# Performance work log

Measured on AMD Instinct MI355X. Metric: run time of the kernel, lower is better.

The kernel has to match this reference:

```python
import jax, jax.numpy as jnp
import numpy as np

T = 37          # bio_type_num
LP = T + 2      # padded label size (start, end)
START, END = T, T + 1


def crf_loglik(logits, labels, lens, trans):
    # logits: [B,S,LP] padded scores; labels: [B,S] ints; lens: [B]; trans[to, from]: [LP,LP]
    B, S, Lp = logits.shape
    dt = logits.dtype
    tpos = jnp.arange(S)
    mask = (tpos[None, :] < lens[:, None]).astype(dt)  # [B,S]
    # unary gold score
    unary = jnp.take_along_axis(logits, labels[..., None], axis=2)[..., 0] * mask
    # binary (transition) gold score with start/end extension
    labels_ext = jnp.concatenate([
        jnp.full((B, 1), START, labels.dtype), labels, jnp.full((B, 1), END, labels.dtype)], axis=1)  # [B,S+2]
    pos = jnp.arange(S + 2)
    labels_ext = jnp.where(pos[None, :] < (lens + 1)[:, None], labels_ext, END)
    frm, to = labels_ext[:, :-1], labels_ext[:, 1:]          # [B,S+1]
    trn_scr = trans[to, frm]                                  # [B,S+1]
    m2 = (jnp.arange(S + 1)[None, :] < (lens + 1)[:, None]).astype(dt)
    gold = unary.sum(1) + (trn_scr * m2).sum(1)               # [B]
    # partition function: forward algorithm (sequential scan over time)
    alpha0 = jnp.full((B, Lp), -100.0, dt).at[:, START].set(0.0)
    def step(alpha, xt):
        logit_t, m_t = xt                                     # [B,Lp], [B] bool
        mat = logit_t[:, :, None] + alpha[:, None, :] + trans[None, :, :]  # [B,to,from]
        alpha_nxt = jax.nn.logsumexp(mat, axis=2)
        alpha = jnp.where(m_t[:, None], alpha_nxt, alpha)
        return alpha, None
    xs = (jnp.swapaxes(logits, 0, 1), (tpos[None, :] < lens[:, None]).T)
    alpha, _ = jax.lax.scan(step, alpha0, xs)
    alpha = alpha + trans[END][None, :]
    norm = jax.nn.logsumexp(alpha, axis=1)                    # [B]
    return gold - norm


def ner_forward(h, bio_embed, W_cat, b_cat, W_crf, b_crf, transition, token_nums, entity_seq_labels):
    B, S, H = h.shape
    scale = 1.0 / jnp.sqrt(jnp.asarray(H, h.dtype))
    # one-head attention: query=token states, key=value=bio type embeddings (mask all ones -> no-op)
    scores = jnp.einsum('bsh,th->bst', h, bio_embed) * scale  # [B,S,T]
    attn = jax.nn.softmax(scores, axis=-1)
    aware = jnp.einsum('bst,th->bsh', attn, bio_embed)        # [B,S,H]
    x = jnp.concatenate([h, aware, h * aware], axis=-1)       # [B,S,3H]
    x = jax.nn.gelu(x @ W_cat + b_cat, approximate=False)     # [B,S,H]
    logits = x @ W_crf + b_crf                                # [B,S,T]
    pads = jnp.full((B, S, 2), -10000.0, logits.dtype)
    ner_scores = jnp.concatenate([logits, pads], axis=-1)     # [B,S,LP]
    ner_loss = crf_loglik(ner_scores, entity_seq_labels, token_nums, transition)
    return ner_scores, ner_loss


def setup_inputs() -> dict:
    key = jax.random.key(0)
    ks = jax.random.split(key, 8)
    B, S, H = 32, 512, 1024
    token_hidden_states = jax.random.normal(ks[0], (B, S, H), jnp.float32)
    token_masks = jnp.ones((B, S), jnp.bool_)
    token_nums = jax.random.randint(ks[1], (B,), 256, S + 1).at[0].set(S)
    entity_seq_labels = jax.random.randint(ks[2], (B, S), 0, T)
    bio_embed = jax.random.normal(ks[3], (T, H), jnp.float32) * 0.02
    W_cat = jax.random.normal(ks[4], (3 * H, H), jnp.float32) * (3.0 * H) ** -0.5
    b_cat = jnp.zeros((H,), jnp.float32)
    W_crf = jax.random.normal(ks[5], (H, T), jnp.float32) * H ** -0.5
    b_crf = jnp.zeros((T,), jnp.float32)
    transition = jax.random.normal(ks[6], (LP, LP), jnp.float32)
    return {
        'token_hidden_states': token_hidden_states, 'token_masks': token_masks,
        'token_nums': token_nums, 'entity_seq_labels': entity_seq_labels,
        'bio_embed': bio_embed, 'W_cat': W_cat, 'b_cat': b_cat,
        'W_crf': W_crf, 'b_crf': b_crf, 'transition': transition,
    }


def reference(token_hidden_states, token_masks, token_nums, entity_seq_labels,
              bio_embed, W_cat, b_cat, W_crf, b_crf, transition):
    # token_masks only generates an all-ones bio mask in the original (no-op); dropout in eval mode.
    return ner_forward(token_hidden_states, bio_embed, W_cat, b_cat, W_crf, b_crf,
                       transition, token_nums, entity_seq_labels)
```

## Files before the change

kernel.cpp:

```cpp
#include <hip/hip_runtime.h>
#include <hip/hip_bf16.h>
#include <math.h>

#define NB 32
#define NS 512
#define NH 1024
#define NT 37
#define NLP 39
#define NM (NB*NS)

typedef __attribute__((ext_vector_type(8))) short bf16x8;
typedef __attribute__((ext_vector_type(4))) float f32x4;

__device__ __forceinline__ float bf2f(unsigned int u) {
    unsigned int x = u << 16;
    float f;
    __builtin_memcpy(&f, &x, 4);
    return f;
}
__device__ __forceinline__ unsigned short f2bf(float f) {
    __hip_bfloat16 hb = __float2bfloat16(f);
    unsigned short u;
    __builtin_memcpy(&u, &hb, 2);
    return u;
}
__device__ __forceinline__ unsigned int pk2(float lo, float hi) {
    return ((unsigned int)f2bf(hi) << 16) | (unsigned int)f2bf(lo);
}
__device__ __forceinline__ int SW64(int b)  { return b ^ ((b >> 2) & 0x70); }
__device__ __forceinline__ int TSW(int row, int kcolByte) {
    return (row * 128 + kcolByte) ^ ((row & 7) << 4);
}
__device__ __forceinline__ float rl(float x, int l) {
    return __int_as_float(__builtin_amdgcn_readlane(__float_as_int(x), l));
}
__device__ __forceinline__ void gld16(const void* g, void* l) {
    __builtin_amdgcn_global_load_lds((const __attribute__((address_space(1))) void*)g,
                                     (__attribute__((address_space(3))) void*)l, 16, 0, 0);
}
#define VMW(N) asm volatile("s_waitcnt vmcnt(" #N ")" ::: "memory")
#define BARR() do { __builtin_amdgcn_s_barrier(); __builtin_amdgcn_sched_barrier(0); } while (0)

__global__ __launch_bounds__(512) void kA1(const float* __restrict__ h,
                                           const float* __restrict__ bio,
                                           unsigned short* __restrict__ attn) {
    __shared__ __align__(16) char Bl[48 * 2048];

    const int tid  = threadIdx.x;
    const int lane = tid & 63;
    const int wid  = tid >> 6;
    const int lr   = lane & 15;
    const int lk   = lane >> 4;
    const int m0   = blockIdx.x * 128;

    for (int idx = tid; idx < 37 * 256; idx += 512) {
        int t = idx >> 8, k4 = idx & 255;
        float4 v = *(const float4*)&bio[(size_t)t * NH + k4 * 4];
        int byte = (t * 2048 + k4 * 8) ^ ((t & 7) << 4);
        *(uint2*)(Bl + byte) = make_uint2(pk2(v.x, v.y), pk2(v.z, v.w));
    }
    for (int idx = tid; idx < 11 * 256; idx += 512) {
        int t = 37 + (idx >> 8), k4 = idx & 255;
        int byte = (t * 2048 + k4 * 8) ^ ((t & 7) << 4);
        *(uint2*)(Bl + byte) = make_uint2(0, 0);
    }
    __syncthreads();

    const int arow = m0 + wid * 16 + lr;
    const float* hp = h + (size_t)arow * NH + lk * 8;

    f32x4 sacc[3];
#pragma unroll
    for (int j = 0; j < 3; ++j) sacc[j] = (f32x4){0.f, 0.f, 0.f, 0.f};

    float4 p0 = *(const float4*)(hp);
    float4 p1 = *(const float4*)(hp + 4);
    for (int kt = 0; kt < NH; kt += 32) {
        float4 c0 = p0, c1 = p1;
        if (kt + 32 < NH) {
            p0 = *(const float4*)(hp + kt + 32);
            p1 = *(const float4*)(hp + kt + 36);
        }
        union { unsigned int u[4]; bf16x8 v; } af;
        af.u[0] = pk2(c0.x, c0.y); af.u[1] = pk2(c0.z, c0.w);
        af.u[2] = pk2(c1.x, c1.y); af.u[3] = pk2(c1.z, c1.w);
#pragma unroll
        for (int nf = 0; nf < 3; ++nf) {
            int t = nf * 16 + lr;
            int byte = (t * 2048 + (kt + lk * 8) * 2) ^ ((t & 7) << 4);
            bf16x8 bf = *(const bf16x8*)(Bl + byte);
            sacc[nf] = __builtin_amdgcn_mfma_f32_16x16x32_bf16(af.v, bf, sacc[nf], 0, 0, 0);
        }
    }

#pragma unroll
    for (int r = 0; r < 4; ++r) {
        const int orow = wid * 16 + lk * 4 + r;
        float s0 = sacc[0][r] * 0.03125f;
        float s1 = sacc[1][r] * 0.03125f;
        float s2 = sacc[2][r] * 0.03125f;
        const bool v2 = (lr < 5);
        float mx = fmaxf(fmaxf(s0, s1), v2 ? s2 : -1e30f);
#pragma unroll
        for (int d = 1; d < 16; d <<= 1) mx = fmaxf(mx, __shfl_xor(mx, d, 64));
        float e0 = __expf(s0 - mx), e1 = __expf(s1 - mx);
        float e2 = v2 ? __expf(s2 - mx) : 0.f;
        float sm = e0 + e1 + e2;
#pragma unroll
        for (int d = 1; d < 16; d <<= 1) sm += __shfl_xor(sm, d, 64);
        float inv = 1.f / sm;
        size_t g = (size_t)(m0 + orow) * 64;
        attn[g + lr]      = f2bf(e0 * inv);
        attn[g + 16 + lr] = f2bf(e1 * inv);
        attn[g + 32 + lr] = f2bf(e2 * inv);
        attn[g + 48 + lr] = 0;
    }
}

__global__ __launch_bounds__(256) void kA2(const unsigned short* __restrict__ attn,
                                           const float* __restrict__ bio,
                                           unsigned short* __restrict__ aware) {
    __shared__ __align__(16) char Bsl[128 * 64];

    const int tid  = threadIdx.x;
    const int lane = tid & 63;
    const int wid  = tid >> 6;
    const int wm   = (wid >> 1) * 64;
    const int wn   = (wid & 1) * 64;
    const int lr   = lane & 15;
    const int lk   = lane >> 4;
    const int n0   = blockIdx.x * 128;
    const int m0   = blockIdx.y * 128;

    const int bn = tid & 127;
    const int bq = (tid >> 7) * 16;

    f32x4 acc[4][4];
#pragma unroll
    for (int i = 0; i < 4; ++i)
#pragma unroll
        for (int j = 0; j < 4; ++j) acc[i][j] = (f32x4){0.f, 0.f, 0.f, 0.f};

#pragma unroll
    for (int ks = 0; ks < 2; ++ks) {
        unsigned int p[8];
#pragma unroll
        for (int i = 0; i < 8; ++i) {
            int t0 = ks*32 + bq + 2*i;
            float lo = (t0     < NT) ? bio[(size_t)t0 * NH + n0 + bn]       : 0.f;
            float hi = (t0 + 1 < NT) ? bio[(size_t)(t0+1) * NH + n0 + bn]   : 0.f;
            p[i] = pk2(lo, hi);
        }
        __syncthreads();
        *(int4*)(Bsl + SW64(bn*64 + bq*2))      = make_int4(p[0], p[1], p[2], p[3]);
        *(int4*)(Bsl + SW64(bn*64 + bq*2 + 16)) = make_int4(p[4], p[5], p[6], p[7]);
        __syncthreads();

        bf16x8 af[4];
#pragma unroll
        for (int mf = 0; mf < 4; ++mf)
            af[mf] = *(const bf16x8*)(attn + (size_t)(m0 + wm + mf*16 + lr) * 64 + ks*32 + lk*8);
#pragma unroll
        for (int nf = 0; nf < 4; ++nf) {
            bf16x8 bb = *(const bf16x8*)(Bsl + SW64((wn + nf*16 + lr)*64 + lk*16));
#pragma unroll
            for (int mf = 0; mf < 4; ++mf)
                acc[mf][nf] = __builtin_amdgcn_mfma_f32_16x16x32_bf16(af[mf], bb, acc[mf][nf], 0, 0, 0);
        }
    }

#pragma unroll
    for (int mf = 0; mf < 4; ++mf)
#pragma unroll
        for (int nf = 0; nf < 4; ++nf)
#pragma unroll
            for (int r = 0; r < 4; ++r) {
                size_t row = (size_t)(m0 + wm + mf*16 + lk*4 + r);
                aware[row * NH + n0 + wn + nf*16 + lr] = f2bf(acc[mf][nf][r]);
            }
}

__global__ __launch_bounds__(256) void kA2f(const unsigned short* __restrict__ attn,
                                            const float* __restrict__ bio,
                                            const float* __restrict__ h,
                                            char* __restrict__ Asw) {
    __shared__ __align__(16) char Bsl[128 * 64];
    __shared__ __align__(16) unsigned short awL[128 * 128];

    const int tid  = threadIdx.x;
    const int lane = tid & 63;
    const int wid  = tid >> 6;
    const int wm   = (wid >> 1) * 64;
    const int wn   = (wid & 1) * 64;
    const int lr   = lane & 15;
    const int lk   = lane >> 4;
    const int n0   = blockIdx.x * 128;
    const int m0   = blockIdx.y * 128;
    const int tm   = blockIdx.y;

    const int bn = tid & 127;
    const int bq = (tid >> 7) * 16;

    f32x4 acc[4][4];
#pragma unroll
    for (int i = 0; i < 4; ++i)
#pragma unroll
        for (int j = 0; j < 4; ++j) acc[i][j] = (f32x4){0.f, 0.f, 0.f, 0.f};

#pragma unroll
    for (int ks = 0; ks < 2; ++ks) {
        unsigned int p[8];
#pragma unroll
        for (int i = 0; i < 8; ++i) {
            int t0 = ks*32 + bq + 2*i;
            float lo = (t0     < NT) ? bio[(size_t)t0 * NH + n0 + bn]       : 0.f;
            float hi = (t0 + 1 < NT) ? bio[(size_t)(t0+1) * NH + n0 + bn]   : 0.f;
            p[i] = pk2(lo, hi);
        }
        __syncthreads();
        *(int4*)(Bsl + SW64(bn*64 + bq*2))      = make_int4(p[0], p[1], p[2], p[3]);
        *(int4*)(Bsl + SW64(bn*64 + bq*2 + 16)) = make_int4(p[4], p[5], p[6], p[7]);
        __syncthreads();

        bf16x8 af[4];
#pragma unroll
        for (int mf = 0; mf < 4; ++mf)
            af[mf] = *(const bf16x8*)(attn + (size_t)(m0 + wm + mf*16 + lr) * 64 + ks*32 + lk*8);
#pragma unroll
        for (int nf = 0; nf < 4; ++nf) {
            bf16x8 bb = *(const bf16x8*)(Bsl + SW64((wn + nf*16 + lr)*64 + lk*16));
#pragma unroll
            for (int mf = 0; mf < 4; ++mf)
                acc[mf][nf] = __builtin_amdgcn_mfma_f32_16x16x32_bf16(af[mf], bb, acc[mf][nf], 0, 0, 0);
        }
    }

#pragma unroll
    for (int mf = 0; mf < 4; ++mf)
#pragma unroll
        for (int nf = 0; nf < 4; ++nf)
#pragma unroll
            for (int r = 0; r < 4; ++r)
                awL[(wm + mf*16 + lk*4 + r) * 128 + wn + nf*16 + lr] = f2bf(acc[mf][nf][r]);
    __syncthreads();

#pragma unroll
    for (int i = 0; i < 8; ++i) {
        int lin = tid + i * 256;
        int row = lin >> 4, kg = lin & 15;
        uint4 v = *(const uint4*)&awL[row * 128 + kg * 8];
        int kglob = 1024 + n0 + kg * 8;
        size_t tbase = ((size_t)tm * 48 + (kglob >> 6)) * 16384;
        *(uint4*)(Asw + tbase + TSW(row, (kglob & 63) * 2)) = v;
    }
#pragma unroll
    for (int i = 0; i < 8; ++i) {
        int lin = tid + i * 256;
        int row = lin >> 4, kg = lin & 15;
        const float4* hp = (const float4*)&h[(size_t)(m0 + row) * NH + n0 + kg * 8];
        float4 ha = hp[0], hb = hp[1];
        float hv[8] = {ha.x, ha.y, ha.z, ha.w, hb.x, hb.y, hb.z, hb.w};
        uint4 awv = *(const uint4*)&awL[row * 128 + kg * 8];
        unsigned int awu[4] = {awv.x, awv.y, awv.z, awv.w};
        unsigned int p0[4], p2[4];
#pragma unroll
        for (int j = 0; j < 4; ++j) {
            p0[j] = pk2(hv[2*j], hv[2*j+1]);
            float lo = hv[2*j]   * bf2f(awu[j] & 0xffffu);
            float hi = hv[2*j+1] * bf2f(awu[j] >> 16);
            p2[j] = pk2(lo, hi);
        }
        int k0g = n0 + kg * 8;
        size_t tb0 = ((size_t)tm * 48 + (k0g >> 6)) * 16384;
        *(uint4*)(Asw + tb0 + TSW(row, (k0g & 63) * 2)) = make_uint4(p0[0], p0[1], p0[2], p0[3]);
        int k2g = 2048 + n0 + kg * 8;
        size_t tb2 = ((size_t)tm * 48 + (k2g >> 6)) * 16384;
        *(uint4*)(Asw + tb2 + TSW(row, (k2g & 63) * 2)) = make_uint4(p2[0], p2[1], p2[2], p2[3]);
    }
}

__global__ __launch_bounds__(256) void kW(const float* __restrict__ Wcat,
                                          char* __restrict__ Wsw) {
    __shared__ unsigned short wt[64 * 128];

    const int tid  = threadIdx.x;
    const int tile = blockIdx.x;
    const int tn   = tile / 48;
    const int tk   = tile - tn * 48;
    const int n00  = tn * 128;
    const int k0   = tk * 64;

#pragma unroll
    for (int i = 0; i < 8; ++i) {
        int lin = tid + i * 256;
        int kk = lin >> 5, ng = lin & 31;
        float4 v = *(const float4*)&Wcat[(size_t)(k0 + kk) * NH + n00 + ng * 4];
        unsigned int lo = pk2(v.x, v.y), hi = pk2(v.z, v.w);
        *(uint2*)&wt[kk * 128 + ng * 4] = make_uint2(lo, hi);
    }
    __syncthreads();
#pragma unroll
    for (int i = 0; i < 4; ++i) {
        int lin = tid + i * 256;
        int rn = lin >> 3, kg = lin & 7;
        unsigned short t8[8];
#pragma unroll
        for (int j = 0; j < 8; ++j) t8[j] = wt[(kg * 8 + j) * 128 + rn];
        uint4 v = *(const uint4*)t8;
        *(uint4*)(Wsw + (size_t)tile * 16384 + TSW(rn, kg * 16)) = v;
    }
}

__global__ __launch_bounds__(256) void kW2(const float* __restrict__ Wcrf,
                                           unsigned short* __restrict__ WT) {
    const int idx = blockIdx.x * 256 + threadIdx.x;
    if (idx >= 48 * 384) return;
    const int t = idx / 384, kg = idx - t * 384;
    unsigned short v[8];
#pragma unroll
    for (int e = 0; e < 8; ++e) {
        int k = kg * 8 + e;
        v[e] = (t < NT) ? f2bf(Wcrf[(size_t)k * NT + t]) : (unsigned short)0;
    }
    uint4 w;
    __builtin_memcpy(&w, v, 16);
    *(uint4*)(WT + (size_t)t * 3072 + kg * 8) = w;
}

__global__ __launch_bounds__(512, 2) void kBf(const char* __restrict__ Asw,
                                              const char* __restrict__ Wsw,
                                              const float* __restrict__ bcat,
                                              const unsigned short* __restrict__ WT,
                                              float* __restrict__ P) {
    __shared__ __align__(16) char lds[131072];

    const int tid  = threadIdx.x;
    const int lane = tid & 63;
    const int wid  = tid >> 6;
    const int widm = wid >> 2;
    const int widn = wid & 3;
    const int lr   = lane & 15;
    const int lk   = lane >> 4;

    const int id   = blockIdx.x;
    const int xcd  = id & 7;
    const int slot = id >> 3;
    const int Mt   = xcd * 8 + (slot >> 2);
    const int Nt   = slot & 3;
    const int m0   = Mt * 256, n0 = Nt * 256;
    const int soff = tid * 16;

    f32x4 acc00[4][2], acc01[4][2], acc10[4][2], acc11[4][2];
#pragma unroll
    for (int i = 0; i < 4; ++i)
#pragma unroll
        for (int j = 0; j < 2; ++j) {
            acc00[i][j] = (f32x4){0.f,0.f,0.f,0.f};
            acc01[i][j] = (f32x4){0.f,0.f,0.f,0.f};
            acc10[i][j] = (f32x4){0.f,0.f,0.f,0.f};
            acc11[i][j] = (f32x4){0.f,0.f,0.f,0.f};
        }

    auto stageHalf = [&](int T, int ph) {
        const bool isA = (ph == 0) || (ph == 3);
        const int  h   = isA ? (ph == 3 ? 1 : 0) : (ph - 1);
        const char* src = isA
            ? Asw + ((size_t)((2*Mt + h) * 48 + T)) * 16384
            : Wsw + ((size_t)((2*Nt + h) * 48 + T)) * 16384;
        char* dst = lds + (isA ? 0 : 65536) + (T & 1) * 32768 + h * 16384;
        gld16(src + soff,        dst + soff);
        gld16(src + soff + 8192, dst + soff + 8192);
    };
    auto loadA = [&](bf16x8 (&af)[4][2], int q, int half) {
        const char* base = lds + q * 32768 + half * 16384;
#pragma unroll
        for (int i = 0; i < 4; ++i) {
            int row = widm * 64 + i * 16 + lr;
#pragma unroll
            for (int kk = 0; kk < 2; ++kk)
                af[i][kk] = *(const bf16x8*)(base + TSW(row, kk * 64 + lk * 16));
        }
    };
    auto loadB = [&](bf16x8 (&bfr)[2][2], int q, int half) {
        const char* base = lds + 65536 + q * 32768 + half * 16384;
#pragma unroll
        for (int j = 0; j < 2; ++j) {
            int col = widn * 32 + j * 16 + lr;
#pragma unroll
            for (int kk = 0; kk < 2; ++kk)
                bfr[j][kk] = *(const bf16x8*)(base + TSW(col, kk * 64 + lk * 16));
        }
    };
    auto mma = [&](f32x4 (&ac)[4][2], bf16x8 (&af)[4][2], bf16x8 (&bfr)[2][2]) {
        __builtin_amdgcn_s_setprio(1);
#pragma unroll
        for (int kk = 0; kk < 2; ++kk)
#pragma unroll
            for (int i = 0; i < 4; ++i)
#pragma unroll
                for (int j = 0; j < 2; ++j)
                    ac[i][j] = __builtin_amdgcn_mfma_f32_16x16x32_bf16(
                        af[i][kk], bfr[j][kk], ac[i][j], 0, 0, 0);
        __builtin_amdgcn_s_setprio(0);
    };

    stageHalf(0, 0); stageHalf(0, 1); stageHalf(0, 2); stageHalf(0, 3);
    VMW(0);
    BARR();

    for (int T = 0; T < 47; ++T) {
        const int q = T & 1;
        bf16x8 af0[4][2], af1[4][2], bf0[2][2], bf1[2][2];
        stageHalf(T + 1, 0);
        VMW(6);
        BARR();
        loadA(af0, q, 0); loadB(bf0, q, 0);
        mma(acc00, af0, bf0);
        stageHalf(T + 1, 1);
        VMW(6);
        BARR();
        loadB(bf1, q, 1);
        mma(acc01, af0, bf1);
        stageHalf(T + 1, 2);
        VMW(6);
        BARR();
        loadA(af1, q, 1);
        mma(acc10, af1, bf0);
        stageHalf(T + 1, 3);
        BARR();
        mma(acc11, af1, bf1);
    }
    {
        const int q = 1;
        bf16x8 af0[4][2], af1[4][2], bf0[2][2], bf1[2][2];
        VMW(4);
        BARR();
        loadA(af0, q, 0); loadB(bf0, q, 0);
        mma(acc00, af0, bf0);
        VMW(2);
        BARR();
        loadB(bf1, q, 1);
        mma(acc01, af0, bf1);
        VMW(0);
        BARR();
        loadA(af1, q, 1);
        mma(acc10, af1, bf0);
        BARR();
        mma(acc11, af1, bf1);
    }

    __syncthreads();
    auto stashQ = [&](f32x4 (&ac)[4][2], int a, int b) {
#pragma unroll
        for (int j = 0; j < 2; ++j) {
            const int lcol = b * 128 + widn * 32 + j * 16 + lr;
            const int kc = lcol >> 6, kk = lcol & 63;
            const float bc = bcat[n0 + lcol];
#pragma unroll
            for (int i = 0; i < 4; ++i)
#pragma unroll
                for (int r = 0; r < 4; ++r) {
                    int lrow = a * 128 + widm * 64 + i * 16 + lk * 4 + r;
                    float x = ac[i][j][r] + bc;
                    float g = 0.5f * x * (1.0f + erff(x * 0.70710678118654752f));
                    *(unsigned short*)(lds + kc * 32768 + TSW(lrow, kk * 2)) = f2bf(g);
                }
        }
    };
    stashQ(acc00, 0, 0); stashQ(acc01, 0, 1); stashQ(acc10, 1, 0); stashQ(acc11, 1, 1);
    __syncthreads();

    bf16x8 wfrag[3][8];
#pragma unroll
    for (int tt = 0; tt < 3; ++tt) {
        const int t = tt * 16 + lr;
#pragma unroll
        for (int ks = 0; ks < 8; ++ks)
            wfrag[tt][ks] = *(const bf16x8*)(WT + (size_t)t * 3072 + n0 + ks * 32 + lk * 8);
    }

    f32x4 pacc[2][3];
#pragma unroll
    for (int i = 0; i < 2; ++i)
#pragma unroll
        for (int j = 0; j < 3; ++j) pacc[i][j] = (f32x4){0.f, 0.f, 0.f, 0.f};
#pragma unroll
    for (int rt2 = 0; rt2 < 2; ++rt2) {
        const int lrow = wid * 32 + rt2 * 16 + lr;
#pragma unroll
        for (int ks = 0; ks < 8; ++ks) {
            const int kc = ks >> 1, kh = ks & 1;
            bf16x8 af = *(const bf16x8*)(lds + kc * 32768 + TSW(lrow, kh * 64 + lk * 16));
#pragma unroll
            for (int tt = 0; tt < 3; ++tt)
                pacc[rt2][tt] = __builtin_amdgcn_mfma_f32_16x16x32_bf16(
                    af, wfrag[tt][ks], pacc[rt2][tt], 0, 0, 0);
        }
    }

    float* Pb = P + (size_t)Nt * NM * 48;
#pragma unroll
    for (int rt2 = 0; rt2 < 2; ++rt2)
#pragma unroll
        for (int tt = 0; tt < 3; ++tt)
#pragma unroll
            for (int r = 0; r < 4; ++r) {
                int row = Mt * 256 + wid * 32 + rt2 * 16 + lk * 4 + r;
                Pb[(size_t)row * 48 + tt * 16 + lr] = pacc[rt2][tt][r];
            }
}

__global__ __launch_bounds__(256) void kCr(const float* __restrict__ P,
                                           const float* __restrict__ bcrf,
                                           float* __restrict__ out) {
    const int g = blockIdx.x * 256 + threadIdx.x;
    const size_t STRIDE = (size_t)NM * 48;
#pragma unroll
    for (int s = 0; s < 12; ++s) {
        int flat = g * 12 + s;
        int row = flat / 48, t = flat - row * 48;
        float v = P[flat] + P[STRIDE + flat] + P[2*STRIDE + flat] + P[3*STRIDE + flat];
        if (t < NT)       out[(size_t)row * NLP + t] = v + bcrf[t];
        else if (t < NLP) out[(size_t)row * NLP + t] = -10000.0f;
    }
}

__global__ __launch_bounds__(64) void kDm(const float* __restrict__ scores,
                                          const int* __restrict__ lens,
                                          const float* __restrict__ trans,
                                          float* __restrict__ Pm,
                                          float* __restrict__ Pc) {
    __shared__ float el_all[64 * 64];
    __shared__ __align__(16) char Mb[2 * 6144];

    const int lane = threadIdx.x;
    const int b    = blockIdx.x >> 3;
    const int s    = blockIdx.x & 7;
    const int lr   = lane & 15;
    const int lk   = lane >> 4;
    const int len  = lens[b];
    const int t0   = s * 64;
    const int nsteps = (len > t0) ? ((len - t0 < 64) ? (len - t0) : 64) : 0;
    const float* sb = scores + (size_t)b * NS * NLP;
    float* Pg = Pm + (size_t)(b * 8 + s) * 2304;

    if (nsteps == 0) {
        for (int j = 0; j < 36; ++j) {
            int flat = j * 64 + lane;
            Pg[flat] = 0.f;
        }
        if (lane < 48) Pg[lane * 48 + lane] = (lane < NLP) ? 1.f : 1.f;
        if (lane == 0) Pc[b * 8 + s] = 0.f;
        return;
    }

    for (int i = 0; i < 64; ++i) {
        float v = 0.f;
        if (i < nsteps && lane < NLP) v = __expf(sb[(size_t)(t0 + i) * NLP + lane]);
        el_all[i * 64 + lane] = v;
    }

    bf16x8 Tf[3][2];
#pragma unroll
    for (int tt = 0; tt < 3; ++tt)
#pragma unroll
        for (int ks = 0; ks < 2; ++ks) {
            const int row = tt * 16 + lr;
            unsigned int u[4];
#pragma unroll
            for (int e2 = 0; e2 < 4; ++e2) {
                int f0 = ks * 32 + lk * 8 + 2 * e2;
                float lo = (row < NLP && f0     < NLP) ? __expf(trans[row * NLP + f0])     : 0.f;
                float hi = (row < NLP && f0 + 1 < NLP) ? __expf(trans[row * NLP + f0 + 1]) : 0.f;
                u[e2] = pk2(lo, hi);
            }
            union { unsigned int uu[4]; bf16x8 v; } cv;
            cv.uu[0]=u[0]; cv.uu[1]=u[1]; cv.uu[2]=u[2]; cv.uu[3]=u[3];
            Tf[tt][ks] = cv.v;
        }

    for (int j = 0; j < 48; ++j)
        *(unsigned int*)(Mb + j * 256 + lane * 4) = 0;
    if (lane < 48) {
        int byte = (lane * 128 + lane * 2) ^ ((lane & 7) << 4);
        *(unsigned short*)(Mb + byte) = f2bf(1.0f);
    }

    float Cacc = 0.f;

    for (int i = 0; i < nsteps; ++i) {
        const int q = i & 1;
        const char* Mr = Mb + q * 6144;

        bf16x8 Bf[3][2];
#pragma unroll
        for (int ct = 0; ct < 3; ++ct) {
#pragma unroll
            for (int ks = 0; ks < 2; ++ks) {
                int col = ct * 16 + lr;
                int byte = (col * 128 + (ks * 32 + lk * 8) * 2) ^ ((col & 7) << 4);
                Bf[ct][ks] = *(const bf16x8*)(Mr + byte);
            }
        }
        f32x4 el4[3];
#pragma unroll
        for (int tt = 0; tt < 3; ++tt)
            el4[tt] = *(const f32x4*)&el_all[i * 64 + tt * 16 + lk * 4];

        f32x4 c[3][3];
#pragma unroll
        for (int tt = 0; tt < 3; ++tt)
#pragma unroll
            for (int ct = 0; ct < 3; ++ct) {
                c[tt][ct] = __builtin_amdgcn_mfma_f32_16x16x32_bf16(
                    Tf[tt][0], Bf[ct][0], (f32x4){0.f,0.f,0.f,0.f}, 0, 0, 0);
                c[tt][ct] = __builtin_amdgcn_mfma_f32_16x16x32_bf16(
                    Tf[tt][1], Bf[ct][1], c[tt][ct], 0, 0, 0);
            }
#pragma unroll
        for (int tt = 0; tt < 3; ++tt)
#pragma unroll
            for (int ct = 0; ct < 3; ++ct)
#pragma unroll
                for (int r = 0; r < 4; ++r)
                    c[tt][ct][r] *= el4[tt][r];

        if ((i & 3) == 3) {
            float sv = rl(c[0][0][0], 0);
            float rr = __builtin_amdgcn_rcpf(sv);
#pragma unroll
            for (int tt = 0; tt < 3; ++tt)
#pragma unroll
                for (int ct = 0; ct < 3; ++ct)
#pragma unroll
                    for (int r = 0; r < 4; ++r) c[tt][ct][r] *= rr;
            Cacc -= __logf(rr);
        }

        if (i == nsteps - 1) {
#pragma unroll
            for (int tt = 0; tt < 3; ++tt)
#pragma unroll
                for (int ct = 0; ct < 3; ++ct)
#pragma unroll
                    for (int r = 0; r < 4; ++r) {
                        int row = tt * 16 + lk * 4 + r;
                        int col = ct * 16 + lr;
                        Pg[row * 48 + col] = c[tt][ct][r];
                    }
        } else {
            char* Mw = Mb + (q ^ 1) * 6144;
#pragma unroll
            for (int tt = 0; tt < 3; ++tt)
#pragma unroll
                for (int ct = 0; ct < 3; ++ct) {
                    int col = ct * 16 + lr;
                    int k   = tt * 16 + lk * 4;
                    int byte = (col * 128 + k * 2) ^ ((col & 7) << 4);
                    *(uint2*)(Mw + byte) = make_uint2(pk2(c[tt][ct][0], c[tt][ct][1]),
                                                      pk2(c[tt][ct][2], c[tt][ct][3]));
                }
        }
    }

    if (lane == 0) Pc[b * 8 + s] = Cacc;
}

__global__ __launch_bounds__(256) void kDc(const float* __restrict__ scores,
                                           const int* __restrict__ labels,
                                           const int* __restrict__ lens,
                                           const float* __restrict__ trans,
                                           const float* __restrict__ Pm,
                                           const float* __restrict__ Pc,
                                           float* __restrict__ loss) {
    __shared__ float trL[39 * 41];
    __shared__ float gred[4];

    const int b    = blockIdx.x;
    const int tid  = threadIdx.x;
    const int lane = tid & 63;
    const int wid  = tid >> 6;
    const int len  = lens[b];
    const float* sb = scores + (size_t)b * NS * NLP;

    for (int idx = tid; idx < 39 * 39; idx += 256) {
        int to = idx / 39, f = idx - to * 39;
        trL[to * 41 + f] = trans[idx];
    }
    __syncthreads();

    float g = 0.0f;
    for (int t = tid; t < len; t += 256) g += sb[(size_t)t * NLP + labels[b * NS + t]];
    for (int i = tid; i <= len; i += 256) {
        int frm = (i == 0) ? 37 : labels[b * NS + i - 1];
        int to  = (i == len) ? 38 : labels[b * NS + i];
        g += trL[to * 41 + frm];
    }
#pragma unroll
    for (int off = 32; off > 0; off >>= 1) g += __shfl_xor(g, off, 64);
    if (lane == 0) gred[wid] = g;
    __syncthreads();

    if (wid != 0) return;

    const float gold = (gred[0] + gred[1]) + (gred[2] + gred[3]);
    const bool act48 = (lane < 48);

    const float* P0 = Pm + (size_t)b * 8 * 2304;
    float v = act48 ? P0[lane * 48 + 37] : 0.f;
    float C = Pc[b * 8];

    for (int s = 1; s < 8; ++s) {
        float as_[40];
#pragma unroll
        for (int f = 0; f < 40; ++f) as_[f] = rl(v, f);
        __builtin_amdgcn_sched_barrier(0);
        const float* Ps = Pm + (size_t)(b * 8 + s) * 2304;
        float c = 0.f;
        if (act48) {
            const float4* rowp = (const float4*)(Ps + lane * 48);
#pragma unroll
            for (int q = 0; q < 10; ++q) {
                float4 rv = rowp[q];
                c = fmaf(rv.x, as_[q*4+0], c);
                c = fmaf(rv.y, as_[q*4+1], c);
                c = fmaf(rv.z, as_[q*4+2], c);
                c = fmaf(rv.w, as_[q*4+3], c);
            }
        }
        float sv = rl(c, 0);
        float rr = __builtin_amdgcn_rcpf(sv);
        v = c * rr;
        C -= __logf(rr);
        C += Pc[b * 8 + s];
    }

    const float trEnd = (lane < NLP) ? trL[38 * 41 + lane] : 0.f;
    float aend = (lane < NLP && v > 0.f) ? C + __logf(v) + trEnd : -1e30f;
    float mx = aend;
#pragma unroll
    for (int off = 32; off > 0; off >>= 1) mx = fmaxf(mx, __shfl_xor(mx, off, 64));
    float es = (lane < NLP) ? __expf(aend - mx) : 0.f;
#pragma unroll
    for (int off = 32; off > 0; off >>= 1) es += __shfl_xor(es, off, 64);
    float norm = mx + __logf(es);

    if (lane == 0) loss[b] = gold - norm;
}

__global__ __launch_bounds__(256) void kB(const float* __restrict__ h,
                                          const unsigned short* __restrict__ aware,
                                          const float* __restrict__ Wcat,
                                          const float* __restrict__ bcat,
                                          unsigned short* __restrict__ x2) {
    __shared__ __align__(16) char lds[16384];
    char* Asl = lds;
    char* Bsl = lds + 8192;

    const int tid  = threadIdx.x;
    const int lane = tid & 63;
    const int wid  = tid >> 6;
    const int wm   = (wid >> 1) * 64;
    const int wn   = (wid & 1) * 64;
    const int lr   = lane & 15;
    const int lk   = lane >> 4;

    const int id   = blockIdx.x;
    const int xcd  = id & 7;
    const int slot = id >> 3;
    const int m0   = (xcd * 16 + (slot >> 3)) * 128;
    const int n0   = (slot & 7) * 128;

    const int am = tid >> 1;
    const int ak = (tid & 1) * 16;
    const int bn = tid & 127;
    const int bk = (tid >> 7) * 16;

    f32x4 acc[4][4];
#pragma unroll
    for (int i = 0; i < 4; ++i)
#pragma unroll
        for (int j = 0; j < 4; ++j) acc[i][j] = (f32x4){0.f, 0.f, 0.f, 0.f};

    const float*          hrow = h     + (size_t)(m0 + am) * NH + ak;
    const unsigned short* arow = aware + (size_t)(m0 + am) * NH + ak;
    const float*          wcol = Wcat  + (size_t)bk * NH + n0 + bn;

    float hv[16];
    unsigned int aw[8];
    float wv[16];

    auto stage = [&](int kt) {
        const int region = kt >> 10;
        const int kb = kt & 1023;
        if (region != 1) {
            const float4* hp = (const float4*)(hrow + kb);
            float4 a = hp[0], b = hp[1], c = hp[2], d = hp[3];
            hv[0]=a.x; hv[1]=a.y; hv[2]=a.z; hv[3]=a.w;
            hv[4]=b.x; hv[5]=b.y; hv[6]=b.z; hv[7]=b.w;
            hv[8]=c.x; hv[9]=c.y; hv[10]=c.z; hv[11]=c.w;
            hv[12]=d.x; hv[13]=d.y; hv[14]=d.z; hv[15]=d.w;
        }
        if (region >= 1) {
            const uint4* ap = (const uint4*)(arow + kb);
            uint4 a0 = ap[0], a1 = ap[1];
            aw[0]=a0.x; aw[1]=a0.y; aw[2]=a0.z; aw[3]=a0.w;
            aw[4]=a1.x; aw[5]=a1.y; aw[6]=a1.z; aw[7]=a1.w;
        }
        {
            const float* wp = wcol + (size_t)kt * NH;
#pragma unroll
            for (int j = 0; j < 16; ++j) wv[j] = wp[(size_t)j * NH];
        }
    };

    auto writeStage = [&](int kt) {
        const int region = kt >> 10;
        unsigned int p[8];
        if (region == 0) {
#pragma unroll
            for (int i = 0; i < 8; ++i) p[i] = pk2(hv[2*i], hv[2*i+1]);
        } else if (region == 1) {
#pragma unroll
            for (int i = 0; i < 8; ++i) p[i] = aw[i];
        } else {
#pragma unroll
            for (int i = 0; i < 8; ++i) {
                float lo = hv[2*i]   * bf2f(aw[i] & 0xffffu);
                float hi = hv[2*i+1] * bf2f(aw[i] >> 16);
                p[i] = pk2(lo, hi);
            }
        }
        *(int4*)(Asl + SW64(am*64 + ak*2))      = make_int4(p[0], p[1], p[2], p[3]);
        *(int4*)(Asl + SW64(am*64 + ak*2 + 16)) = make_int4(p[4], p[5], p[6], p[7]);
        unsigned int q[8];
#pragma unroll
        for (int i = 0; i < 8; ++i) q[i] = pk2(wv[2*i], wv[2*i+1]);
        *(int4*)(Bsl + SW64(bn*64 + bk*2))      = make_int4(q[0], q[1], q[2], q[3]);
        *(int4*)(Bsl + SW64(bn*64 + bk*2 + 16)) = make_int4(q[4], q[5], q[6], q[7]);
    };

    stage(0);
    for (int kt = 0; kt < 3072; kt += 32) {
        __syncthreads();
        writeStage(kt);
        __syncthreads();
        if (kt + 32 < 3072) stage(kt + 32);

        bf16x8 af[4], bfr[4];
#pragma unroll
        for (int mf = 0; mf < 4; ++mf)
            af[mf] = *(const bf16x8*)(Asl + SW64((wm + mf*16 + lr)*64 + lk*16));
#pragma unroll
        for (int nf = 0; nf < 4; ++nf)
            bfr[nf] = *(const bf16x8*)(Bsl + SW64((wn + nf*16 + lr)*64 + lk*16));
#pragma unroll
        for (int mf = 0; mf < 4; ++mf)
#pragma unroll
            for (int nf = 0; nf < 4; ++nf)
                acc[mf][nf] = __builtin_amdgcn_mfma_f32_16x16x32_bf16(af[mf], bfr[nf], acc[mf][nf], 0, 0, 0);
    }

#pragma unroll
    for (int nf = 0; nf < 4; ++nf) {
        const int col = n0 + wn + nf*16 + lr;
        const float bc = bcat[col];
#pragma unroll
        for (int mf = 0; mf < 4; ++mf)
#pragma unroll
            for (int r = 0; r < 4; ++r) {
                size_t row = (size_t)(m0 + wm + mf*16 + lk*4 + r);
                float x = acc[mf][nf][r] + bc;
                float g = 0.5f * x * (1.0f + erff(x * 0.70710678118654752f));
                x2[row * NH + col] = f2bf(g);
            }
    }
}

__global__ __launch_bounds__(256) void kC(const unsigned short* __restrict__ x2,
                                          const float* __restrict__ Wcrf,
                                          const float* __restrict__ bcrf,
                                          float* __restrict__ out) {
    __shared__ __align__(16) char Asl[8192];
    __shared__ __align__(16) char Bsl[3072];

    const int tid  = threadIdx.x;
    const int lane = tid & 63;
    const int wid  = tid >> 6;
    const int lr   = lane & 15;
    const int lk   = lane >> 4;
    const int m0   = blockIdx.x * 128;
    const int am   = tid >> 1;
    const int ak   = (tid & 1) * 16;

    for (int i = tid; i < 192; i += 256) *(int4*)(Bsl + i*16) = make_int4(0, 0, 0, 0);

    f32x4 acc[2][3];
#pragma unroll
    for (int i = 0; i < 2; ++i)
#pragma unroll
        for (int j = 0; j < 3; ++j) acc[i][j] = (f32x4){0.f, 0.f, 0.f, 0.f};

    const unsigned short* xrow = x2 + (size_t)(m0 + am) * NH + ak;

    for (int kt = 0; kt < NH; kt += 32) {
        const uint4* xp = (const uint4*)(xrow + kt);
        uint4 x0 = xp[0], x1 = xp[1];
        float wv[5];
#pragma unroll
        for (int p = 0; p < 5; ++p) {
            int i = tid + p * 256;
            wv[p] = (i < 32*NT) ? Wcrf[(size_t)kt * NT + i] : 0.f;
        }
        __syncthreads();
        *(uint4*)(Asl + SW64(am*64 + ak*2))      = x0;
        *(uint4*)(Asl + SW64(am*64 + ak*2 + 16)) = x1;
#pragma unroll
        for (int p = 0; p < 5; ++p) {
            int i = tid + p * 256;
            if (i < 32*NT) {
                int kk = i / NT;
                int t  = i - kk * NT;
                *(unsigned short*)(Bsl + SW64(t*64 + kk*2)) = f2bf(wv[p]);
            }
        }
        __syncthreads();
        bf16x8 af[2], bfr[3];
#pragma unroll
        for (int mf = 0; mf < 2; ++mf)
            af[mf] = *(const bf16x8*)(Asl + SW64((wid*32 + mf*16 + lr)*64 + lk*16));
#pragma unroll
        for (int nf = 0; nf < 3; ++nf)
            bfr[nf] = *(const bf16x8*)(Bsl + SW64((nf*16 + lr)*64 + lk*16));
#pragma unroll
        for (int mf = 0; mf < 2; ++mf)
#pragma unroll
            for (int nf = 0; nf < 3; ++nf)
                acc[mf][nf] = __builtin_amdgcn_mfma_f32_16x16x32_bf16(af[mf], bfr[nf], acc[mf][nf], 0, 0, 0);
    }

#pragma unroll
    for (int nf = 0; nf < 3; ++nf) {
        const int t = nf*16 + lr;
        const float bc = (t < NT) ? bcrf[t] : 0.f;
#pragma unroll
        for (int mf = 0; mf < 2; ++mf)
#pragma unroll
            for (int r = 0; r < 4; ++r) {
                size_t row = (size_t)(m0 + wid*32 + mf*16 + lk*4 + r);
                if (t < NT)       out[row * NLP + t] = acc[mf][nf][r] + bc;
                else if (t < NLP) out[row * NLP + t] = -10000.0f;
            }
    }
}

#define CRFSTEP(EL) do {                                   \
    float as_[37];                                         \
    _Pragma("unroll")                                      \
    for (int f_ = 0; f_ < 37; ++f_) as_[f_] = rl(a, f_);   \
    __builtin_amdgcn_sched_barrier(0);                     \
    float c0 = 0.f, c1 = 0.f, c2 = 0.f, c3 = 0.f;          \
    _Pragma("unroll")                                      \
    for (int f_ = 0; f_ < 36; f_ += 4) {                   \
        c0 = fmaf(as_[f_    ], trow[f_    ], c0);          \
        c1 = fmaf(as_[f_ + 1], trow[f_ + 1], c1);          \
        c2 = fmaf(as_[f_ + 2], trow[f_ + 2], c2);          \
        c3 = fmaf(as_[f_ + 3], trow[f_ + 3], c3);          \
    }                                                      \
    c0 = fmaf(as_[36], trow[36], c0);                      \
    a = (EL) * ((c0 + c1) + (c2 + c3));                    \
} while (0)

__global__ __launch_bounds__(256) void kDold(const float* __restrict__ scores,
                                             const int* __restrict__ labels,
                                             const int* __restrict__ lens,
                                             const float* __restrict__ trans,
                                             float* __restrict__ loss) {
    __shared__ float S[NS * NLP];
    __shared__ float trL[39 * 41];
    __shared__ int   labL[NS];
    __shared__ float gred[4];

    const int b    = blockIdx.x;
    const int tid  = threadIdx.x;
    const int lane = tid & 63;
    const int wid  = tid >> 6;
    const int len  = lens[b];
    const float* sb = scores + (size_t)b * NS * NLP;

    {
        const int n4 = (len * NLP + 3) >> 2;
        const float4* src = (const float4*)sb;
        float4* dst = (float4*)S;
        for (int i = tid; i < n4; i += 256) dst[i] = src[i];
    }
    for (int i = tid; i < NS; i += 256) labL[i] = labels[b * NS + i];
    for (int idx = tid; idx < 39 * 39; idx += 256) {
        int to = idx / 39, f = idx - to * 39;
        trL[to * 41 + f] = trans[idx];
    }
    __syncthreads();

    float g = 0.0f;
    for (int t = tid; t < len; t += 256) g += S[t * NLP + labL[t]];
    for (int i = tid; i <= len; i += 256) {
        int frm = (i == 0) ? 37 : labL[i - 1];
        int to  = (i == len) ? 38 : labL[i];
        g += trL[to * 41 + frm];
    }
#pragma unroll
    for (int off = 32; off > 0; off >>= 1) g += __shfl_xor(g, off, 64);
    if (lane == 0) gred[wid] = g;
    __syncthreads();

    if (wid != 0) return;

    const float gold = (gred[0] + gred[1]) + (gred[2] + gred[3]);

    const int myrow = (lane < 39) ? lane : 0;
    float trow[39];
#pragma unroll
    for (int f = 0; f < 39; ++f) trow[f] = __expf(trL[myrow * 41 + f]);
    const float trEnd = (lane < 39) ? trL[38 * 41 + lane] : 0.f;
    const bool act = (lane < 39);

    float l0 = act ? S[lane] : -10000.f;
    float a = act ? __expf(l0) * trow[37] : 0.f;
    float C = 0.0f;

    auto ldrow = [&](int r) {
        r = (r < len) ? r : (len - 1);
        return S[act ? (r * NLP + lane) : 0];
    };
    float lg0 = ldrow(1), lg1 = ldrow(2), lg2 = ldrow(3), lg3 = ldrow(4);

    int t = 1;
    for (; t + 3 < len; t += 4) {
        float e0 = __expf(lg0), e1 = __expf(lg1), e2 = __expf(lg2), e3 = __expf(lg3);
        lg0 = ldrow(t + 4); lg1 = ldrow(t + 5); lg2 = ldrow(t + 6); lg3 = ldrow(t + 7);
        CRFSTEP(e0); CRFSTEP(e1); CRFSTEP(e2); CRFSTEP(e3);
        float s = rl(a, 0);
        float rr = __builtin_amdgcn_rcpf(s);
        a *= rr; C -= __logf(rr);
    }
    for (; t < len; ++t) {
        float el = __expf(ldrow(t));
        CRFSTEP(el);
    }

    float aend = (act && a > 0.f) ? C + __logf(a) + trEnd : -1e30f;
    float mx = aend;
#pragma unroll
    for (int off = 32; off > 0; off >>= 1) mx = fmaxf(mx, __shfl_xor(mx, off, 64));
    float es = act ? __expf(aend - mx) : 0.0f;
#pragma unroll
    for (int off = 32; off > 0; off >>= 1) es += __shfl_xor(es, off, 64);
    float norm = mx + __logf(es);

    if (lane == 0) loss[b] = gold - norm;
}

extern "C" void kernel_launch(void* const* d_in, const int* in_sizes, int n_in,
                              void* d_out, int out_size, void* d_ws, size_t ws_size,
                              hipStream_t stream) {
    const float* h        = (const float*)d_in[0];
    const int* token_nums = (const int*)d_in[2];
    const int* labels     = (const int*)d_in[3];
    const float* bio      = (const float*)d_in[4];
    const float* Wcat     = (const float*)d_in[5];
    const float* bcat     = (const float*)d_in[6];
    const float* Wcrf     = (const float*)d_in[7];
    const float* bcrf     = (const float*)d_in[8];
    const float* trans    = (const float*)d_in[9];

    float* out = (float*)d_out;
    unsigned short* attn  = (unsigned short*)d_out;

    const size_t ASW_BYTES = (size_t)128 * 48 * 16384;
    const size_t P_BYTES   = (size_t)4 * NM * 48 * 4;
    const size_t WSW_BYTES = (size_t)8 * 48 * 16384;
    const size_t WT_BYTES  = (size_t)48 * 3072 * 2;
    const size_t PM_BYTES  = (size_t)NB * 8 * 2304 * 4;
    const size_t PC_BYTES  = (size_t)NB * 8 * 4;
    const bool fast = ws_size >= ASW_BYTES + P_BYTES + WSW_BYTES + WT_BYTES + PM_BYTES + PC_BYTES;

    hipLaunchKernelGGL(kA1, dim3(NM / 128), dim3(512), 0, stream, h, bio, attn);

    if (fast) {
        char*  Asw = (char*)d_ws;
        float* P   = (float*)((char*)d_ws + ASW_BYTES);
        char*  Wsw = (char*)d_ws + ASW_BYTES + P_BYTES;
        unsigned short* WT = (unsigned short*)((char*)d_ws + ASW_BYTES + P_BYTES + WSW_BYTES);
        float* Pm  = (float*)((char*)d_ws + ASW_BYTES + P_BYTES + WSW_BYTES + WT_BYTES);
        float* Pc  = Pm + (size_t)NB * 8 * 2304;

        hipLaunchKernelGGL(kW, dim3(8 * 48), dim3(256), 0, stream, Wcat, Wsw);
        hipLaunchKernelGGL(kW2, dim3(72), dim3(256), 0, stream, Wcrf, WT);
        hipLaunchKernelGGL(kA2f, dim3(NH / 128, NM / 128), dim3(256), 0, stream,
                           attn, bio, h, Asw);
        hipLaunchKernelGGL(kBf, dim3(256), dim3(512), 0, stream, Asw, Wsw, bcat, WT, P);
        hipLaunchKernelGGL(kCr, dim3(256), dim3(256), 0, stream, P, bcrf, out);
        hipLaunchKernelGGL(kDm, dim3(NB * 8), dim3(64), 0, stream, out, token_nums, trans,
                           Pm, Pc);
        hipLaunchKernelGGL(kDc, dim3(NB), dim3(256), 0, stream, out, labels, token_nums,
                           trans, Pm, Pc, out + (size_t)NM * NLP);
    } else {
        unsigned short* aware = (unsigned short*)d_ws;
        unsigned short* x2    = aware + (size_t)NM * NH;

        hipLaunchKernelGGL(kA2, dim3(NH / 128, NM / 128), dim3(256), 0, stream, attn, bio, aware);
        hipLaunchKernelGGL(kB, dim3((NH / 128) * (NM / 128)), dim3(256), 0, stream,
                           h, aware, Wcat, bcat, x2);
        hipLaunchKernelGGL(kC, dim3(NM / 128), dim3(256), 0, stream, x2, Wcrf, bcrf, out);
        hipLaunchKernelGGL(kDold, dim3(NB), dim3(256), 0, stream, out, labels, token_nums,
                           trans, out + (size_t)NM * NLP);
    }
}
```

Measured before the change: 244.7 us.

## Merge attention-score, weight-prep kernels into one launch and reuse bf16 h from workspace

Three launches (attention-score softmax, Wcat swizzle, Wcrf transpose) become one kernel, kPre, that picks its role from the block index. The score part also writes the bf16 copy of h into the swizzled A workspace while it streams h. kA2f then reads that bf16 copy instead of reloading fp32 h, which removes one full fp32 read of h and two launches. The h*aware product is now formed from bf16-rounded h rather than fp32 h, which changes rounding slightly.

```diff
diff --git a/kernel.cpp b/kernel.cpp
--- a/kernel.cpp
+++ b/kernel.cpp
@@ -40,6 +40,134 @@
 }
 #define VMW(N) asm volatile("s_waitcnt vmcnt(" #N ")" ::: "memory")
 #define BARR() do { __builtin_amdgcn_s_barrier(); __builtin_amdgcn_sched_barrier(0); } while (0)
+
+__global__ __launch_bounds__(512) void kPre(const float* __restrict__ h,
+                                            const float* __restrict__ bio,
+                                            const float* __restrict__ Wcat,
+                                            const float* __restrict__ Wcrf,
+                                            unsigned short* __restrict__ attn,
+                                            char* __restrict__ Asw,
+                                            char* __restrict__ Wsw,
+                                            unsigned short* __restrict__ WT) {
+    __shared__ __align__(16) char shmem[48 * 2048];
+    const int bid = blockIdx.x;
+    const int tid = threadIdx.x;
+
+    if (bid < 128) {
+        char* Bl = shmem;
+        const int lane = tid & 63;
+        const int wid  = tid >> 6;
+        const int lr   = lane & 15;
+        const int lk   = lane >> 4;
+        const int m0   = bid * 128;
+
+        for (int idx = tid; idx < 37 * 256; idx += 512) {
+            int t = idx >> 8, k4 = idx & 255;
+            float4 v = *(const float4*)&bio[(size_t)t * NH + k4 * 4];
+            int byte = (t * 2048 + k4 * 8) ^ ((t & 7) << 4);
+            *(uint2*)(Bl + byte) = make_uint2(pk2(v.x, v.y), pk2(v.z, v.w));
+        }
+        for (int idx = tid; idx < 11 * 256; idx += 512) {
+            int t = 37 + (idx >> 8), k4 = idx & 255;
+            int byte = (t * 2048 + k4 * 8) ^ ((t & 7) << 4);
+            *(uint2*)(Bl + byte) = make_uint2(0, 0);
+        }
+        __syncthreads();
+
+        const int arow = m0 + wid * 16 + lr;
+        const float* hp = h + (size_t)arow * NH + lk * 8;
+        const int trow = wid * 16 + lr;
+
+        f32x4 sacc[3];
+#pragma unroll
+        for (int j = 0; j < 3; ++j) sacc[j] = (f32x4){0.f, 0.f, 0.f, 0.f};
+
+        float4 p0 = *(const float4*)(hp);
+        float4 p1 = *(const float4*)(hp + 4);
+        for (int kt = 0; kt < NH; kt += 32) {
+            float4 c0 = p0, c1 = p1;
+            if (kt + 32 < NH) {
+                p0 = *(const float4*)(hp + kt + 32);
+                p1 = *(const float4*)(hp + kt + 36);
+            }
+            union { unsigned int u[4]; bf16x8 v; uint4 q; } af;
+            af.u[0] = pk2(c0.x, c0.y); af.u[1] = pk2(c0.z, c0.w);
+            af.u[2] = pk2(c1.x, c1.y); af.u[3] = pk2(c1.z, c1.w);
+            {
+                int kg = kt + lk * 8;
+                size_t tb = ((size_t)bid * 48 + (kg >> 6)) * 16384;
+                *(uint4*)(Asw + tb + TSW(trow, (kg & 63) * 2)) = af.q;
+            }
+#pragma unroll
+            for (int nf = 0; nf < 3; ++nf) {
+                int t = nf * 16 + lr;
+                int byte = (t * 2048 + (kt + lk * 8) * 2) ^ ((t & 7) << 4);
+                bf16x8 bf = *(const bf16x8*)(Bl + byte);
+                sacc[nf] = __builtin_amdgcn_mfma_f32_16x16x32_bf16(af.v, bf, sacc[nf], 0, 0, 0);
+            }
+        }
+
+#pragma unroll
+        for (int r = 0; r < 4; ++r) {
+            const int orow = wid * 16 + lk * 4 + r;
+            float s0 = sacc[0][r] * 0.03125f;
+            float s1 = sacc[1][r] * 0.03125f;
+            float s2 = sacc[2][r] * 0.03125f;
+            const bool v2 = (lr < 5);
+            float mx = fmaxf(fmaxf(s0, s1), v2 ? s2 : -1e30f);
+#pragma unroll
+            for (int d = 1; d < 16; d <<= 1) mx = fmaxf(mx, __shfl_xor(mx, d, 64));
+            float e0 = __expf(s0 - mx), e1 = __expf(s1 - mx);
+            float e2 = v2 ? __expf(s2 - mx) : 0.f;
+            float sm = e0 + e1 + e2;
+#pragma unroll
+            for (int d = 1; d < 16; d <<= 1) sm += __shfl_xor(sm, d, 64);
+            float inv = 1.f / sm;
+            size_t g = (size_t)(m0 + orow) * 64;
+            attn[g + lr]      = f2bf(e0 * inv);
+            attn[g + 16 + lr] = f2bf(e1 * inv);
+            attn[g + 32 + lr] = f2bf(e2 * inv);
+            attn[g + 48 + lr] = 0;
+        }
+    } else if (bid < 512) {
+        unsigned short* wt = (unsigned short*)shmem;
+        const int tile = bid - 128;
+        const int tn   = tile / 48;
+        const int tk   = tile - tn * 48;
+        const int n00  = tn * 128;
+        const int k0   = tk * 64;
+
+        for (int lin = tid; lin < 2048; lin += 512) {
+            int kk = lin >> 5, ng = lin & 31;
+            float4 v = *(const float4*)&Wcat[(size_t)(k0 + kk) * NH + n00 + ng * 4];
+            *(uint2*)&wt[kk * 128 + ng * 4] = make_uint2(pk2(v.x, v.y), pk2(v.z, v.w));
+        }
+        __syncthreads();
+        for (int lin = tid; lin < 1024; lin += 512) {
+            int rn = lin >> 3, kg = lin & 7;
+            unsigned short t8[8];
+#pragma unroll
+            for (int j = 0; j < 8; ++j) t8[j] = wt[(kg * 8 + j) * 128 + rn];
+            uint4 v;
+            __builtin_memcpy(&v, t8, 16);
+            *(uint4*)(Wsw + (size_t)tile * 16384 + TSW(rn, kg * 16)) = v;
+        }
+    } else {
+        const int idx = (bid - 512) * 512 + tid;
+        if (idx < 48 * 384) {
+            const int t = idx / 384, kg = idx - t * 384;
+            unsigned short v[8];
+#pragma unroll
+            for (int e = 0; e < 8; ++e) {
+                int k = kg * 8 + e;
+                v[e] = (t < NT) ? f2bf(Wcrf[(size_t)k * NT + t]) : (unsigned short)0;
+            }
+            uint4 w;
+            __builtin_memcpy(&w, v, 16);
+            *(uint4*)(WT + (size_t)t * 3072 + kg * 8) = w;
+        }
+    }
+}
 
 __global__ __launch_bounds__(512) void kA1(const float* __restrict__ h,
                                            const float* __restrict__ bio,
@@ -182,7 +310,6 @@
 
 __global__ __launch_bounds__(256) void kA2f(const unsigned short* __restrict__ attn,
                                             const float* __restrict__ bio,
-                                            const float* __restrict__ h,
                                             char* __restrict__ Asw) {
     __shared__ __align__(16) char Bsl[128 * 64];
     __shared__ __align__(16) unsigned short awL[128 * 128];
@@ -257,75 +384,25 @@
     for (int i = 0; i < 8; ++i) {
         int lin = tid + i * 256;
         int row = lin >> 4, kg = lin & 15;
-        const float4* hp = (const float4*)&h[(size_t)(m0 + row) * NH + n0 + kg * 8];
-        float4 ha = hp[0], hb = hp[1];
-        float hv[8] = {ha.x, ha.y, ha.z, ha.w, hb.x, hb.y, hb.z, hb.w};
+        int k0g = n0 + kg * 8;
+        size_t tb0 = ((size_t)tm * 48 + (k0g >> 6)) * 16384;
+        uint4 hv4 = *(const uint4*)(Asw + tb0 + TSW(row, (k0g & 63) * 2));
+        unsigned int hu[4] = {hv4.x, hv4.y, hv4.z, hv4.w};
         uint4 awv = *(const uint4*)&awL[row * 128 + kg * 8];
         unsigned int awu[4] = {awv.x, awv.y, awv.z, awv.w};
-        unsigned int p0[4], p2[4];
+        unsigned int p2[4];
 #pragma unroll
         for (int j = 0; j < 4; ++j) {
-            p0[j] = pk2(hv[2*j], hv[2*j+1]);
-            float lo = hv[2*j]   * bf2f(awu[j] & 0xffffu);
-            float hi = hv[2*j+1] * bf2f(awu[j] >> 16);
+            float lo = bf2f(hu[j] & 0xffffu) * bf2f(awu[j] & 0xffffu);
+            float hi = bf2f(hu[j] >> 16)     * bf2f(awu[j] >> 16);
             p2[j] = pk2(lo, hi);
         }
-        int k0g = n0 + kg * 8;
-        size_t tb0 = ((size_t)tm * 48 + (k0g >> 6)) * 16384;
-        *(uint4*)(Asw + tb0 + TSW(row, (k0g & 63) * 2)) = make_uint4(p0[0], p0[1], p0[2], p0[3]);
         int k2g = 2048 + n0 + kg * 8;
         size_t tb2 = ((size_t)tm * 48 + (k2g >> 6)) * 16384;
         *(uint4*)(Asw + tb2 + TSW(row, (k2g & 63) * 2)) = make_uint4(p2[0], p2[1], p2[2], p2[3]);
     }
 }
 
-__global__ __launch_bounds__(256) void kW(const float* __restrict__ Wcat,
-                                          char* __restrict__ Wsw) {
-    __shared__ unsigned short wt[64 * 128];
-
-    const int tid  = threadIdx.x;
-    const int tile = blockIdx.x;
-    const int tn   = tile / 48;
-    const int tk   = tile - tn * 48;
-    const int n00  = tn * 128;
-    const int k0   = tk * 64;
-
-#pragma unroll
-    for (int i = 0; i < 8; ++i) {
-        int lin = tid + i * 256;
-        int kk = lin >> 5, ng = lin & 31;
-        float4 v = *(const float4*)&Wcat[(size_t)(k0 + kk) * NH + n00 + ng * 4];
-        unsigned int lo = pk2(v.x, v.y), hi = pk2(v.z, v.w);
-        *(uint2*)&wt[kk * 128 + ng * 4] = make_uint2(lo, hi);
-    }
-    __syncthreads();
-#pragma unroll
-    for (int i = 0; i < 4; ++i) {
-        int lin = tid + i * 256;
-        int rn = lin >> 3, kg = lin & 7;
-        unsigned short t8[8];
-#pragma unroll
-        for (int j = 0; j < 8; ++j) t8[j] = wt[(kg * 8 + j) * 128 + rn];
-        uint4 v = *(const uint4*)t8;
-        *(uint4*)(Wsw + (size_t)tile * 16384 + TSW(rn, kg * 16)) = v;
-    }
-}
-
-__global__ __launch_bounds__(256) void kW2(const float* __restrict__ Wcrf,
-                                           unsigned short* __restrict__ WT) {
-    const int idx = blockIdx.x * 256 + threadIdx.x;
-    if (idx >= 48 * 384) return;
-    const int t = idx / 384, kg = idx - t * 384;
-    unsigned short v[8];
-#pragma unroll
-    for (int e = 0; e < 8; ++e) {
-        int k = kg * 8 + e;
-        v[e] = (t < NT) ? f2bf(Wcrf[(size_t)k * NT + t]) : (unsigned short)0;
-    }
-    uint4 w;
-    __builtin_memcpy(&w, v, 16);
-    *(uint4*)(WT + (size_t)t * 3072 + kg * 8) = w;
-}
 
 __global__ __launch_bounds__(512, 2) void kBf(const char* __restrict__ Asw,
                                               const char* __restrict__ Wsw,
@@ -545,11 +622,8 @@
     float* Pg = Pm + (size_t)(b * 8 + s) * 2304;
 
     if (nsteps == 0) {
-        for (int j = 0; j < 36; ++j) {
-            int flat = j * 64 + lane;
-            Pg[flat] = 0.f;
-        }
-        if (lane < 48) Pg[lane * 48 + lane] = (lane < NLP) ? 1.f : 1.f;
+        for (int j = 0; j < 36; ++j) Pg[j * 64 + lane] = 0.f;
+        if (lane < 48) Pg[lane * 48 + lane] = 1.f;
         if (lane == 0) Pc[b * 8 + s] = 0.f;
         return;
     }
@@ -1084,8 +1158,6 @@
     const size_t PC_BYTES  = (size_t)NB * 8 * 4;
     const bool fast = ws_size >= ASW_BYTES + P_BYTES + WSW_BYTES + WT_BYTES + PM_BYTES + PC_BYTES;
 
-    hipLaunchKernelGGL(kA1, dim3(NM / 128), dim3(512), 0, stream, h, bio, attn);
-
     if (fast) {
         char*  Asw = (char*)d_ws;
         float* P   = (float*)((char*)d_ws + ASW_BYTES);
@@ -1094,10 +1166,10 @@
         float* Pm  = (float*)((char*)d_ws + ASW_BYTES + P_BYTES + WSW_BYTES + WT_BYTES);
         float* Pc  = Pm + (size_t)NB * 8 * 2304;
 
-        hipLaunchKernelGGL(kW, dim3(8 * 48), dim3(256), 0, stream, Wcat, Wsw);
-        hipLaunchKernelGGL(kW2, dim3(72), dim3(256), 0, stream, Wcrf, WT);
+        hipLaunchKernelGGL(kPre, dim3(548), dim3(512), 0, stream,
+                           h, bio, Wcat, Wcrf, attn, Asw, Wsw, WT);
         hipLaunchKernelGGL(kA2f, dim3(NH / 128, NM / 128), dim3(256), 0, stream,
-                           attn, bio, h, Asw);
+                           attn, bio, Asw);
         hipLaunchKernelGGL(kBf, dim3(256), dim3(512), 0, stream, Asw, Wsw, bcat, WT, P);
         hipLaunchKernelGGL(kCr, dim3(256), dim3(256), 0, stream, P, bcrf, out);
         hipLaunchKernelGGL(kDm, dim3(NB * 8), dim3(64), 0, stream, out, token_nums, trans,
@@ -1108,6 +1180,7 @@
         unsigned short* aware = (unsigned short*)d_ws;
         unsigned short* x2    = aware + (size_t)NM * NH;
 
+        hipLaunchKernelGGL(kA1, dim3(NM / 128), dim3(512), 0, stream, h, bio, attn);
         hipLaunchKernelGGL(kA2, dim3(NH / 128, NM / 128), dim3(256), 0, stream, attn, bio, aware);
         hipLaunchKernelGGL(kB, dim3((NH / 128) * (NM / 128)), dim3(256), 0, stream,
                            h, aware, Wcat, bcat, x2);
```

New measurement: 226.5 us (median of 2 runs). 7.5% less time.
